# Optimization experiments

Measured on AMD Instinct MI355X. Metric: run time of the kernel, lower is better.

## Reference

```python
import jax, jax.numpy as jnp
import numpy as np

N = 50000      # nodes
E = 800000     # edges
IN = 32        # raw node feature dim
PE = 15        # laplacian PE dim (k)
HID = 128      # hidden
HEADS = 4
C = HID // HEADS
G = 64         # graphs in batch
L = 4          # num layers (shared weights!)


def setup_inputs() -> dict:
    key = jax.random.key(0)
    ks = jax.random.split(key, 24)
    s = 0.05
    p = lambda k, shape: jax.random.normal(k, shape, dtype=jnp.float32) * s
    inp = {
        "x": jax.random.normal(ks[0], (N, IN), dtype=jnp.float32),
        "edge_index": jax.random.randint(ks[1], (2, E), 0, N, dtype=jnp.int32),
        "batch": jnp.sort(jax.random.randint(ks[2], (N,), 0, G, dtype=jnp.int32)),
        "lap_pe": jax.random.normal(ks[3], (N, PE), dtype=jnp.float32),
        # node_in: Linear(IN+PE -> HID)
        "node_in_w": p(ks[4], (HID, IN + PE)), "node_in_b": p(ks[5], (HID,)),
        # shared TransformerConv params
        "Wq": p(ks[6], (HID, HID)), "bq": p(ks[7], (HID,)),
        "Wk": p(ks[8], (HID, HID)), "bk": p(ks[9], (HID,)),
        "Wv": p(ks[10], (HID, HID)), "bv": p(ks[11], (HID,)),
        "Wskip": p(ks[12], (HID, HID)), "bskip": p(ks[13], (HID,)),
        "Wbeta": p(ks[14], (1, 3 * HID)),  # bias=False in PyG
        # attentional aggregation gate: Linear(HID,HID)->ReLU->Linear(HID,1)
        "g1_w": p(ks[15], (HID, HID)), "g1_b": p(ks[16], (HID,)),
        "g2_w": p(ks[17], (1, HID)), "g2_b": p(ks[18], (1,)),
        # readout: Linear(HID,HID)->ReLU->Linear(HID,1)
        "r1_w": p(ks[19], (HID, HID)), "r1_b": p(ks[20], (HID,)),
        "r2_w": p(ks[21], (1, HID)), "r2_b": p(ks[22], (1,)),
    }
    return inp


def _transformer_conv(x, src, dst, Wq, bq, Wk, bk, Wv, bv, Wskip, bskip, Wbeta):
    # projections -> [N, HEADS, C]
    q = (x @ Wq.T + bq).reshape(N, HEADS, C)
    k = (x @ Wk.T + bk).reshape(N, HEADS, C)
    v = (x @ Wv.T + bv).reshape(N, HEADS, C)
    # edge attention logits: [E, HEADS]
    alpha = jnp.einsum('ehc,ehc->eh', q[dst], k[src]) / jnp.sqrt(jnp.float32(C))
    # segment softmax over destination node
    amax = jax.ops.segment_max(alpha, dst, num_segments=N)        # [N, HEADS]
    ex = jnp.exp(alpha - amax[dst])
    denom = jax.ops.segment_sum(ex, dst, num_segments=N)          # [N, HEADS]
    attn = ex / denom[dst]                                        # [E, HEADS]
    # weighted scatter-add of values
    msg = v[src] * attn[:, :, None]                               # [E, HEADS, C]
    out = jax.ops.segment_sum(msg, dst, num_segments=N).reshape(N, HID)
    # beta-gated skip connection (beta=True, root_weight=True)
    x_r = x @ Wskip.T + bskip
    beta = jax.nn.sigmoid(jnp.concatenate([out, x_r, out - x_r], axis=-1) @ Wbeta.T)
    return beta * x_r + (1.0 - beta) * out


def reference(x, edge_index, batch, lap_pe, node_in_w, node_in_b,
              Wq, bq, Wk, bk, Wv, bv, Wskip, bskip, Wbeta,
              g1_w, g1_b, g2_w, g2_b, r1_w, r1_b, r2_w, r2_b):
    src, dst = edge_index[0], edge_index[1]
    h = jnp.concatenate([x, lap_pe], axis=-1) @ node_in_w.T + node_in_b  # [N, HID]
    for _ in range(L):  # same conv instance reused -> shared weights
        h = jax.nn.relu(h + _transformer_conv(h, src, dst, Wq, bq, Wk, bk,
                                              Wv, bv, Wskip, bskip, Wbeta))
    # attentional aggregation over graphs
    gate = jax.nn.relu(h @ g1_w.T + g1_b) @ g2_w.T + g2_b                # [N, 1]
    gmax = jax.ops.segment_max(gate, batch, num_segments=G)
    gex = jnp.exp(gate - gmax[batch])
    gden = jax.ops.segment_sum(gex, batch, num_segments=G)
    w = gex / gden[batch]                                                # [N, 1]
    g = jax.ops.segment_sum(w * h, batch, num_segments=G)                # [G, HID]
    out = jax.nn.relu(g @ r1_w.T + r1_b) @ r2_w.T + r2_b                 # [G, 1]
    return out.squeeze(-1)
```

## Files before the change

kernel.cpp:

```cpp
#include <hip/hip_runtime.h>

#define NN 50000
#define EE 800000
#define INF 32
#define PEF 15
#define HID 128
#define GG 64
#define NLAYERS 4
#define NBLK 196

typedef __bf16 bf16;
typedef __attribute__((ext_vector_type(8))) bf16 bf16x8;
typedef __attribute__((ext_vector_type(4))) float f32x4;
typedef __attribute__((ext_vector_type(2))) float f32x2;

__device__ __forceinline__ float wave_allsum(float v) {
  #pragma unroll
  for (int off = 1; off < 64; off <<= 1) v += __shfl_xor(v, off);
  return v;
}

__device__ __forceinline__ float bflo(unsigned u) {
  return __builtin_bit_cast(float, u << 16);
}
__device__ __forceinline__ float bfhi(unsigned u) {
  return __builtin_bit_cast(float, u & 0xffff0000u);
}
__device__ __forceinline__ unsigned short f2bf(float v) {
  unsigned b = __builtin_bit_cast(unsigned, v);
  unsigned r = (b + 0x7fffu + ((b >> 16) & 1u)) >> 16;
  return (unsigned short)r;
}
__device__ __forceinline__ unsigned bfpack(float lo, float hi) {
  return (unsigned)f2bf(lo) | ((unsigned)f2bf(hi) << 16);
}
__device__ __forceinline__ unsigned fp8pack4(float a, float b, float c, float d) {
  unsigned lo = (unsigned)__builtin_amdgcn_cvt_pk_fp8_f32(a, b, 0, false) & 0xffffu;
  unsigned hi = (unsigned)__builtin_amdgcn_cvt_pk_fp8_f32(c, d, 0, false) & 0xffffu;
  return lo | (hi << 16);
}

__global__ void pack_weights_kernel(const float* __restrict__ Wq, const float* __restrict__ Wk,
                                    const float* __restrict__ Wv, const float* __restrict__ Ws,
                                    const float* __restrict__ bq, const float* __restrict__ bk,
                                    const float* __restrict__ bv, const float* __restrict__ bs,
                                    unsigned short* __restrict__ Wcatb, float* __restrict__ bcat) {
  int idx = blockIdx.x * blockDim.x + threadIdx.x;
  if (idx >= 512 * 128) return;
  int o = idx >> 7, j = idx & 127;
  int w = o >> 7, r = o & 127;
  const float* W = (w == 0) ? Wq : (w == 1) ? Wk : (w == 2) ? Wv : Ws;
  Wcatb[idx] = f2bf(W[r * 128 + j]);
  if (j == 0) {
    const float* b = (w == 0) ? bq : (w == 1) ? bk : (w == 2) ? bv : bs;
    bcat[o] = b[r];
  }
}

__global__ void pack_nwt_kernel(const float* __restrict__ niw, float* __restrict__ nwT) {
  int idx = blockIdx.x * blockDim.x + threadIdx.x;
  if (idx >= 47 * 128) return;
  int j = idx >> 7, o = idx & 127;
  nwT[j * 128 + o] = niw[o * 47 + j];
}

__global__ void pack_g1_kernel(const float* __restrict__ g1w, unsigned short* __restrict__ g1wb) {
  int idx = blockIdx.x * blockDim.x + threadIdx.x;
  if (idx >= 128 * 128) return;
  g1wb[idx] = f2bf(g1w[idx]);
}

__global__ __launch_bounds__(256) void nodein_kernel(const float* __restrict__ x,
    const float* __restrict__ pe, const float* __restrict__ nwT,
    const float* __restrict__ bias, float* __restrict__ h,
    unsigned short* __restrict__ hbf) {
  int wv = blockIdx.x * 4 + (threadIdx.x >> 6);
  if (wv >= NN) return;
  int lane = threadIdx.x & 63;
  float acc0 = bias[lane], acc1 = bias[64 + lane];
  const float* xr = x + (size_t)wv * INF;
  const float* pr = pe + (size_t)wv * PEF;
  #pragma unroll
  for (int j = 0; j < INF; j++) {
    float f = xr[j];
    acc0 += f * nwT[j * 128 + lane];
    acc1 += f * nwT[j * 128 + 64 + lane];
  }
  #pragma unroll
  for (int j = 0; j < PEF; j++) {
    float f = pr[j];
    acc0 += f * nwT[(INF + j) * 128 + lane];
    acc1 += f * nwT[(INF + j) * 128 + 64 + lane];
  }
  h[(size_t)wv * 128 + lane] = acc0;
  h[(size_t)wv * 128 + 64 + lane] = acc1;
  hbf[(size_t)wv * 128 + lane] = f2bf(acc0);
  hbf[(size_t)wv * 128 + 64 + lane] = f2bf(acc1);
}

__global__ void count_kernel(const int* __restrict__ dst, int* __restrict__ counts) {
  int e = blockIdx.x * blockDim.x + threadIdx.x;
  if (e >= EE) return;
  atomicAdd(&counts[dst[e]], 1);
}

__global__ __launch_bounds__(256) void bsum_kernel(const int* __restrict__ counts,
                                                   int* __restrict__ bsum) {
  int b = blockIdx.x, t = threadIdx.x;
  int i = b * 256 + t;
  int v = (i < NN) ? counts[i] : 0;
  #pragma unroll
  for (int off = 1; off < 64; off <<= 1) v += __shfl_xor(v, off);
  __shared__ int red[4];
  if ((t & 63) == 0) red[t >> 6] = v;
  __syncthreads();
  if (t == 0) bsum[b] = red[0] + red[1] + red[2] + red[3];
}

__global__ void bscan_kernel(const int* __restrict__ bsum, int* __restrict__ bbase) {
  int lane = threadIdx.x;
  int carry = 0;
  for (int c = 0; c < NBLK; c += 64) {
    int i = c + lane;
    int v = (i < NBLK) ? bsum[i] : 0;
    int x = v;
    #pragma unroll
    for (int off = 1; off < 64; off <<= 1) {
      int u = __shfl_up(x, off);
      if (lane >= off) x += u;
    }
    if (i < NBLK) bbase[i] = carry + x - v;
    carry += __shfl(x, 63);
  }
}

__global__ __launch_bounds__(256) void rowptr_kernel(const int* __restrict__ counts,
    const int* __restrict__ bbase, int* __restrict__ row_ptr, int* __restrict__ cursor) {
  int b = blockIdx.x, t = threadIdx.x;
  int lane = t & 63, wid = t >> 6;
  int i = b * 256 + t;
  int v = (i < NN) ? counts[i] : 0;
  int x = v;
  #pragma unroll
  for (int off = 1; off < 64; off <<= 1) {
    int u = __shfl_up(x, off);
    if (lane >= off) x += u;
  }
  __shared__ int wsum[4];
  if (lane == 63) wsum[wid] = x;
  __syncthreads();
  int offs = bbase[b];
  for (int k = 0; k < wid; k++) offs += wsum[k];
  int incl = offs + x;
  if (i < NN) { row_ptr[i + 1] = incl; cursor[i] = incl - v; }
  if (b == 0 && t == 0) row_ptr[0] = 0;
}

__global__ void scatter_kernel(const int* __restrict__ src, const int* __restrict__ dst,
                               int* __restrict__ cursor, int* __restrict__ srcs) {
  int e = blockIdx.x * blockDim.x + threadIdx.x;
  if (e >= EE) return;
  int d = dst[e];
  int p = atomicAdd(&cursor[d], 1);
  srcs[p] = src[e];
}

__global__ void gptr_kernel(const int* __restrict__ batch, int* __restrict__ gptr) {
  int g = threadIdx.x;
  if (g > GG) return;
  if (g == GG) { gptr[GG] = NN; return; }
  int lo = 0, hi = NN;
  while (lo < hi) {
    int mid = (lo + hi) >> 1;
    if (batch[mid] < g) lo = mid + 1; else hi = mid;
  }
  gptr[g] = lo;
}

__global__ __launch_bounds__(256) void gemm0_kernel(
    const bf16* __restrict__ A, const bf16* __restrict__ B,
    const float* __restrict__ bias, int M,
    unsigned short* __restrict__ qbb, unsigned char* __restrict__ kvb,
    unsigned short* __restrict__ xrbb) {
  __shared__ float lds[128 * 64];
  const int t = threadIdx.x;
  const int w = t >> 6, lane = t & 63;
  const int m0 = blockIdx.x * 128;
  const int by = blockIdx.y;
  const int n0 = by * 64;
  const int lrow = lane & 15, lk = (lane >> 4) * 8;
  int ra = m0 + w * 32 + lrow;      if (ra > M - 1) ra = M - 1;
  int rb = m0 + w * 32 + 16 + lrow; if (rb > M - 1) rb = M - 1;
  const bf16* a0p = A + (size_t)ra * 128 + lk;
  const bf16* a1p = A + (size_t)rb * 128 + lk;
  const bf16* bp  = B + (size_t)(n0 + lrow) * 128 + lk;
  f32x4 acc[2][4] = {};
  #pragma unroll
  for (int ks = 0; ks < 4; ks++) {
    bf16x8 a0 = *(const bf16x8*)(a0p + ks * 32);
    bf16x8 a1 = *(const bf16x8*)(a1p + ks * 32);
    #pragma unroll
    for (int nj = 0; nj < 4; nj++) {
      bf16x8 b = *(const bf16x8*)(bp + (size_t)nj * 2048 + ks * 32);
      acc[0][nj] = __builtin_amdgcn_mfma_f32_16x16x32_bf16(a0, b, acc[0][nj], 0, 0, 0);
      acc[1][nj] = __builtin_amdgcn_mfma_f32_16x16x32_bf16(a1, b, acc[1][nj], 0, 0, 0);
    }
  }
  const int rbase = (lane >> 4) * 4;
  #pragma unroll
  for (int mi = 0; mi < 2; mi++) {
    #pragma unroll
    for (int nj = 0; nj < 4; nj++) {
      #pragma unroll
      for (int r = 0; r < 4; r++) {
        int ml = w * 32 + mi * 16 + rbase + r;
        int col = nj * 16 + lrow;
        lds[ml * 64 + (col ^ ((ml & 7) << 2))] = acc[mi][nj][r] + bias[n0 + col];
      }
    }
  }
  __syncthreads();
  #pragma unroll
  for (int kk = 0; kk < 2; kk++) {
    int u = t + kk * 256;
    int r = u & 127, s = u >> 7;
    int m = m0 + r;
    float ff[16];
    #pragma unroll
    for (int j = 0; j < 4; j++) {
      int c = s * 16 + j * 4;
      *(float4*)(ff + j * 4) = *(const float4*)(lds + r * 64 + (c ^ ((r & 7) << 2)));
    }
    if (m < M) {
      int c0 = (by & 1) * 64 + s * 16;
      if (by < 2) {
        unsigned o[8];
        #pragma unroll
        for (int i = 0; i < 8; i++) o[i] = bfpack(ff[2 * i], ff[2 * i + 1]);
        uint4* dst = (uint4*)(qbb + (size_t)m * 128 + c0);
        dst[0] = *(uint4*)&o[0];
        dst[1] = *(uint4*)&o[4];
      } else if (by < 6) {
        unsigned o[4];
        #pragma unroll
        for (int i = 0; i < 4; i++)
          o[i] = fp8pack4(ff[4 * i], ff[4 * i + 1], ff[4 * i + 2], ff[4 * i + 3]);
        int cell = c0 >> 3;
        int voff = (by < 4) ? 0 : 8;
        unsigned char* bp8 = kvb + (size_t)m * 256;
        uint2 w0; w0.x = o[0]; w0.y = o[1];
        uint2 w1; w1.x = o[2]; w1.y = o[3];
        *(uint2*)(bp8 + cell * 16 + voff) = w0;
        *(uint2*)(bp8 + (cell + 1) * 16 + voff) = w1;
      } else {
        unsigned o[8];
        #pragma unroll
        for (int i = 0; i < 8; i++) o[i] = bfpack(ff[2 * i], ff[2 * i + 1]);
        uint4* dst = (uint4*)(xrbb + (size_t)m * 128 + c0);
        dst[0] = *(uint4*)&o[0];
        dst[1] = *(uint4*)&o[4];
      }
    }
  }
}

__global__ __launch_bounds__(512) void gemm1_gate_kernel(
    const bf16* __restrict__ A, const bf16* __restrict__ B,
    const float* __restrict__ b1, const float* __restrict__ g2w,
    const float* __restrict__ g2b, int M, float* __restrict__ gx) {
  const int w = threadIdx.x >> 6, lane = threadIdx.x & 63;
  const int m0 = blockIdx.x * 128 + w * 16;
  const int lrow = lane & 15, lk = (lane >> 4) * 8;
  int ra = m0 + lrow; if (ra > M - 1) ra = M - 1;
  const bf16* ap = A + (size_t)ra * 128 + lk;
  const bf16* bp = B + (size_t)lrow * 128 + lk;
  f32x4 acc[8] = {};
  #pragma unroll
  for (int ks = 0; ks < 4; ks++) {
    bf16x8 a = *(const bf16x8*)(ap + ks * 32);
    #pragma unroll
    for (int nj = 0; nj < 8; nj++) {
      bf16x8 b = *(const bf16x8*)(bp + (size_t)nj * 2048 + ks * 32);
      acc[nj] = __builtin_amdgcn_mfma_f32_16x16x32_bf16(a, b, acc[nj], 0, 0, 0);
    }
  }
  float g2v[8], b1v[8];
  #pragma unroll
  for (int nj = 0; nj < 8; nj++) {
    g2v[nj] = g2w[nj * 16 + lrow];
    b1v[nj] = b1[nj * 16 + lrow];
  }
  const float b2 = g2b[0];
  const int rbase = (lane >> 4) * 4;
  #pragma unroll
  for (int r = 0; r < 4; r++) {
    int m = m0 + rbase + r;
    float d = 0.f;
    #pragma unroll
    for (int nj = 0; nj < 8; nj++)
      d += fmaxf(acc[nj][r] + b1v[nj], 0.f) * g2v[nj];
    d += __shfl_xor(d, 1);
    d += __shfl_xor(d, 2);
    d += __shfl_xor(d, 4);
    d += __shfl_xor(d, 8);
    if (lrow == 0 && m < M) gx[m] = __expf(d + b2);
  }
}

__global__ __launch_bounds__(256) void attn_beta_kernel(
    const unsigned short* __restrict__ qbb,
    const unsigned char* __restrict__ kvb,
    const int* __restrict__ row_ptr, const int* __restrict__ srcs,
    const unsigned* __restrict__ xrb4,
    const float* __restrict__ Wbeta,
    float* __restrict__ h, unsigned* __restrict__ hbf4) {
  __shared__ float xlds[4][128];
  const int wid = threadIdx.x >> 6;
  const int wv = blockIdx.x * 4 + wid;
  const int lane = threadIdx.x & 63;
  const int sl = lane & 15;
  const int eg = lane >> 4;
  float qf[8];
  {
    bf16x8 qv = *(const bf16x8*)((const bf16*)qbb + (size_t)wv * 128 + sl * 8);
    #pragma unroll
    for (int j = 0; j < 8; j++) qf[j] = (float)qv[j];
  }
  const int e0 = row_ptr[wv], e1 = row_ptr[wv + 1];
  const float C = 0.25503486f;
  float dex = 0.f;
  float acc[8] = {0, 0, 0, 0, 0, 0, 0, 0};

#define PROC(cell, valid)                                                   \
  {                                                                         \
    f32x2 k0 = __builtin_amdgcn_cvt_pk_f32_fp8((cell).x, false);            \
    f32x2 k1 = __builtin_amdgcn_cvt_pk_f32_fp8((cell).x, true);             \
    f32x2 k2 = __builtin_amdgcn_cvt_pk_f32_fp8((cell).y, false);            \
    f32x2 k3 = __builtin_amdgcn_cvt_pk_f32_fp8((cell).y, true);             \
    float p = qf[0] * k0.x + qf[1] * k0.y + qf[2] * k1.x + qf[3] * k1.y     \
            + qf[4] * k2.x + qf[5] * k2.y + qf[6] * k3.x + qf[7] * k3.y;    \
    p += __shfl_xor(p, 1);                                                  \
    p += __shfl_xor(p, 2);                                                  \
    float ex = (valid) ? exp2f(p * C) : 0.f;                                \
    dex += ex;                                                              \
    f32x2 v0 = __builtin_amdgcn_cvt_pk_f32_fp8((cell).z, false);            \
    f32x2 v1 = __builtin_amdgcn_cvt_pk_f32_fp8((cell).z, true);             \
    f32x2 v2 = __builtin_amdgcn_cvt_pk_f32_fp8((cell).w, false);            \
    f32x2 v3 = __builtin_amdgcn_cvt_pk_f32_fp8((cell).w, true);             \
    acc[0] += ex * v0.x; acc[1] += ex * v0.y;                               \
    acc[2] += ex * v1.x; acc[3] += ex * v1.y;                               \
    acc[4] += ex * v2.x; acc[5] += ex * v2.y;                               \
    acc[6] += ex * v3.x; acc[7] += ex * v3.y;                               \
  }

  for (int base = e0; base < e1; base += 64) {
    int rem = e1 - base;
    int cnt = rem < 64 ? rem : 64;
    int mysrc = (lane < rem) ? srcs[base + lane] : 0;
    int i = 0;
    for (; i + 4 < cnt; i += 8) {
      int sea = __shfl(mysrc, i + eg);
      int seb = __shfl(mysrc, i + 4 + eg);
      uint4 ca = *(const uint4*)(kvb + (size_t)sea * 256 + sl * 16);
      uint4 cb = *(const uint4*)(kvb + (size_t)seb * 256 + sl * 16);
      PROC(ca, true);
      PROC(cb, (i + 4 + eg < cnt));
    }
    if (i < cnt) {
      int sea = __shfl(mysrc, i + eg);
      uint4 ca = *(const uint4*)(kvb + (size_t)sea * 256 + sl * 16);
      PROC(ca, (i + eg < cnt));
    }
  }
#undef PROC

  dex += __shfl_xor(dex, 16);
  dex += __shfl_xor(dex, 32);
  #pragma unroll
  for (int j = 0; j < 8; j++) {
    acc[j] += __shfl_xor(acc[j], 16);
    acc[j] += __shfl_xor(acc[j], 32);
  }
  float inv = (e1 > e0) ? 1.f / dex : 0.f;
  if (eg == 0) {
    #pragma unroll
    for (int j = 0; j < 8; j++) xlds[wid][sl * 8 + j] = acc[j] * inv;
  }
  __syncthreads();
  float ox = xlds[wid][2 * lane];
  float oy = xlds[wid][2 * lane + 1];
  unsigned xu = xrb4[(size_t)wv * 64 + lane];
  float xx = bflo(xu), xy = bfhi(xu);
  const float2* wb = (const float2*)Wbeta;
  float2 wo = wb[lane], wx = wb[64 + lane], wd = wb[128 + lane];
  float part = ox * wo.x + oy * wo.y + xx * wx.x + xy * wx.y
             + (ox - xx) * wd.x + (oy - xy) * wd.y;
  part = wave_allsum(part);
  float beta = 1.f / (1.f + __expf(-part));
  float2* hp = (float2*)(h + (size_t)wv * 128);
  float2 h2 = hp[lane];
  float r0 = fmaxf(h2.x + beta * xx + (1.f - beta) * ox, 0.f);
  float r1 = fmaxf(h2.y + beta * xy + (1.f - beta) * oy, 0.f);
  h2.x = r0; h2.y = r1;
  hp[lane] = h2;
  hbf4[(size_t)wv * 64 + lane] = bfpack(r0, r1);
}

__global__ __launch_bounds__(256) void gden_kernel(const float* __restrict__ gx,
    const int* __restrict__ gptr, float* __restrict__ gden) {
  int g = blockIdx.x, t = threadIdx.x;
  int n0 = gptr[g], n1 = gptr[g + 1];
  float s = 0.f;
  for (int n = n0 + t; n < n1; n += 256) s += gx[n];
  s = wave_allsum(s);
  __shared__ float red[4];
  if ((t & 63) == 0) red[t >> 6] = s;
  __syncthreads();
  if (t == 0) gden[g] = red[0] + red[1] + red[2] + red[3];
}

__global__ __launch_bounds__(128) void gagg_kernel(const float* __restrict__ gx,
    const float* __restrict__ h, const int* __restrict__ gptr,
    float* __restrict__ gfeat_raw) {
  int g = blockIdx.x;
  int c = blockIdx.y;
  int d = threadIdx.x;
  int n0 = gptr[g], n1 = gptr[g + 1];
  float acc = 0.f;
  for (int n = n0 + c; n < n1; n += 32) acc += gx[n] * h[(size_t)n * 128 + d];
  atomicAdd(&gfeat_raw[g * 128 + d], acc);
}

__global__ __launch_bounds__(128) void readout_kernel(const float* __restrict__ gfeat_raw,
    const float* __restrict__ gden,
    const float* __restrict__ r1w, const float* __restrict__ r1b,
    const float* __restrict__ r2w, const float* __restrict__ r2b,
    float* __restrict__ out) {
  int g = blockIdx.x;
  int u = threadIdx.x;
  __shared__ float sh[128];
  __shared__ float red[128];
  float dv = gden[g];
  float inv = (dv > 0.f) ? 1.f / dv : 0.f;
  sh[u] = gfeat_raw[g * 128 + u] * inv;
  __syncthreads();
  float tacc = r1b[u];
  for (int j = 0; j < 128; j++) tacc += sh[j] * r1w[u * 128 + j];
  tacc = fmaxf(tacc, 0.f);
  red[u] = tacc * r2w[u];
  __syncthreads();
  for (int off = 64; off > 0; off >>= 1) {
    if (u < off) red[u] += red[u + off];
    __syncthreads();
  }
  if (u == 0) out[g] = red[0] + r2b[0];
}

extern "C" void kernel_launch(void* const* d_in, const int* in_sizes, int n_in,
                              void* d_out, int out_size, void* d_ws, size_t ws_size,
                              hipStream_t stream) {
  (void)in_sizes; (void)n_in; (void)out_size; (void)ws_size;
  const float* x     = (const float*)d_in[0];
  const int*   ei    = (const int*)d_in[1];
  const int*   batch = (const int*)d_in[2];
  const float* pe    = (const float*)d_in[3];
  const float* niw   = (const float*)d_in[4];
  const float* nib   = (const float*)d_in[5];
  const float* Wq    = (const float*)d_in[6];
  const float* bq    = (const float*)d_in[7];
  const float* Wk    = (const float*)d_in[8];
  const float* bk    = (const float*)d_in[9];
  const float* Wv    = (const float*)d_in[10];
  const float* bv    = (const float*)d_in[11];
  const float* Wsk   = (const float*)d_in[12];
  const float* bsk   = (const float*)d_in[13];
  const float* Wbeta = (const float*)d_in[14];
  const float* g1w   = (const float*)d_in[15];
  const float* g1b   = (const float*)d_in[16];
  const float* g2w   = (const float*)d_in[17];
  const float* g2b   = (const float*)d_in[18];
  const float* r1w   = (const float*)d_in[19];
  const float* r1b   = (const float*)d_in[20];
  const float* r2w   = (const float*)d_in[21];
  const float* r2b   = (const float*)d_in[22];
  float* out = (float*)d_out;

  float* ws = (float*)d_ws;
  float* h     = ws; ws += (size_t)NN * 128;
  float* qbbf  = ws; ws += (size_t)NN * 64;
  float* kvbf  = ws; ws += (size_t)NN * 64;
  float* xrbf  = ws; ws += (size_t)NN * 64;
  float* hbff  = ws; ws += (size_t)NN * 64;
  float* Wcatf = ws; ws += 512 * 64;
  float* g1wbf = ws; ws += 128 * 64;
  float* bcat  = ws; ws += 512;
  float* nwT   = ws; ws += 47 * 128;
  float* gx    = ws; ws += NN;
  float* gfeat = ws; ws += GG * 128;
  float* gden  = ws; ws += GG;
  int* row_ptr = (int*)ws;
  int* counts  = row_ptr + (NN + 1);
  int* cursor  = counts + NN;
  int* srcs    = cursor + NN;
  int* gptr    = srcs + EE;
  int* bsum    = gptr + (GG + 1);
  int* bbase   = bsum + 256;

  unsigned short* qbb   = (unsigned short*)qbbf;
  unsigned char*  kvb   = (unsigned char*)kvbf;
  unsigned short* xrbb  = (unsigned short*)xrbf;
  unsigned short* hbf   = (unsigned short*)hbff;
  unsigned short* Wcatb = (unsigned short*)Wcatf;
  unsigned short* g1wb  = (unsigned short*)g1wbf;
  const int* src = ei;
  const int* dst = ei + EE;

  hipMemsetAsync(counts, 0, NN * sizeof(int), stream);
  hipMemsetAsync(gfeat, 0, GG * 128 * sizeof(float), stream);
  pack_weights_kernel<<<(512 * 128 + 255) / 256, 256, 0, stream>>>(
      Wq, Wk, Wv, Wsk, bq, bk, bv, bsk, Wcatb, bcat);
  pack_nwt_kernel<<<(47 * 128 + 255) / 256, 256, 0, stream>>>(niw, nwT);
  pack_g1_kernel<<<(128 * 128 + 255) / 256, 256, 0, stream>>>(g1w, g1wb);
  nodein_kernel<<<12500, 256, 0, stream>>>(x, pe, nwT, nib, h, hbf);
  count_kernel<<<(EE + 255) / 256, 256, 0, stream>>>(dst, counts);
  bsum_kernel<<<NBLK, 256, 0, stream>>>(counts, bsum);
  bscan_kernel<<<1, 64, 0, stream>>>(bsum, bbase);
  rowptr_kernel<<<NBLK, 256, 0, stream>>>(counts, bbase, row_ptr, cursor);
  scatter_kernel<<<(EE + 255) / 256, 256, 0, stream>>>(src, dst, cursor, srcs);
  gptr_kernel<<<1, 128, 0, stream>>>(batch, gptr);

  const int MB0 = (NN + 127) / 128;
  for (int l = 0; l < NLAYERS; l++) {
    gemm0_kernel<<<dim3(MB0, 8), 256, 0, stream>>>(
        (const bf16*)hbf, (const bf16*)Wcatb, bcat, NN, qbb, kvb, xrbb);
    attn_beta_kernel<<<12500, 256, 0, stream>>>(
        qbb, kvb, row_ptr, srcs, (const unsigned*)xrbb, Wbeta, h, (unsigned*)hbf);
  }

  gemm1_gate_kernel<<<MB0, 512, 0, stream>>>(
      (const bf16*)hbf, (const bf16*)g1wb, g1b, g2w, g2b, NN, gx);
  gden_kernel<<<GG, 256, 0, stream>>>(gx, gptr, gden);
  gagg_kernel<<<dim3(GG, 32), 128, 0, stream>>>(gx, h, gptr, gfeat);
  readout_kernel<<<GG, 128, 0, stream>>>(gfeat, gden, r1w, r1b, r2w, r2b, out);
}
```

Before: 581.5 us.

## Replace scalar node-input projection with packed bf16 MFMA GEMM

The per-node scalar FMA projection of concatenated raw features and positional encodings is replaced by two kernels. One packs x and lap_pe into a zero-padded 64-wide bf16 row per node, and one runs an MFMA 16x16x32 GEMM against a padded bf16 weight matrix. The GEMM stages results through swizzled LDS so it can write coalesced fp32 h and bf16 hbf. This removes per-lane redundant weight loads and scalar FMAs. In exchange it adds an extra kernel and an intermediate buffer, and it drops the projection inputs from fp32 to bf16 precision.

```diff
diff --git a/kernel.cpp b/kernel.cpp
--- a/kernel.cpp
+++ b/kernel.cpp
@@ -57,11 +57,11 @@
   }
 }
 
-__global__ void pack_nwt_kernel(const float* __restrict__ niw, float* __restrict__ nwT) {
+__global__ void pack_nwtb_kernel(const float* __restrict__ niw, unsigned short* __restrict__ nwtb) {
   int idx = blockIdx.x * blockDim.x + threadIdx.x;
-  if (idx >= 47 * 128) return;
-  int j = idx >> 7, o = idx & 127;
-  nwT[j * 128 + o] = niw[o * 47 + j];
+  if (idx >= 128 * 64) return;
+  int n = idx >> 6, j = idx & 63;
+  nwtb[idx] = (j < INF + PEF) ? f2bf(niw[n * (INF + PEF) + j]) : (unsigned short)0;
 }
 
 __global__ void pack_g1_kernel(const float* __restrict__ g1w, unsigned short* __restrict__ g1wb) {
@@ -70,32 +70,96 @@
   g1wb[idx] = f2bf(g1w[idx]);
 }
 
-__global__ __launch_bounds__(256) void nodein_kernel(const float* __restrict__ x,
-    const float* __restrict__ pe, const float* __restrict__ nwT,
-    const float* __restrict__ bias, float* __restrict__ h,
-    unsigned short* __restrict__ hbf) {
-  int wv = blockIdx.x * 4 + (threadIdx.x >> 6);
-  if (wv >= NN) return;
-  int lane = threadIdx.x & 63;
-  float acc0 = bias[lane], acc1 = bias[64 + lane];
-  const float* xr = x + (size_t)wv * INF;
-  const float* pr = pe + (size_t)wv * PEF;
-  #pragma unroll
-  for (int j = 0; j < INF; j++) {
-    float f = xr[j];
-    acc0 += f * nwT[j * 128 + lane];
-    acc1 += f * nwT[j * 128 + 64 + lane];
-  }
-  #pragma unroll
-  for (int j = 0; j < PEF; j++) {
-    float f = pr[j];
-    acc0 += f * nwT[(INF + j) * 128 + lane];
-    acc1 += f * nwT[(INF + j) * 128 + 64 + lane];
-  }
-  h[(size_t)wv * 128 + lane] = acc0;
-  h[(size_t)wv * 128 + 64 + lane] = acc1;
-  hbf[(size_t)wv * 128 + lane] = f2bf(acc0);
-  hbf[(size_t)wv * 128 + 64 + lane] = f2bf(acc1);
+__global__ __launch_bounds__(256) void xpe_pack_kernel(const float* __restrict__ x,
+    const float* __restrict__ pe, unsigned* __restrict__ xpeb4) {
+  int n = blockIdx.x * 256 + threadIdx.x;
+  if (n >= NN) return;
+  unsigned ou[32];
+  const float4* xr = (const float4*)(x + (size_t)n * INF);
+  #pragma unroll
+  for (int i = 0; i < 8; i++) {
+    float4 v = xr[i];
+    ou[2 * i] = bfpack(v.x, v.y);
+    ou[2 * i + 1] = bfpack(v.z, v.w);
+  }
+  const float* pr = pe + (size_t)n * PEF;
+  float p[16];
+  #pragma unroll
+  for (int i = 0; i < PEF; i++) p[i] = pr[i];
+  p[15] = 0.f;
+  #pragma unroll
+  for (int i = 0; i < 8; i++) ou[16 + i] = bfpack(p[2 * i], p[2 * i + 1]);
+  #pragma unroll
+  for (int i = 24; i < 32; i++) ou[i] = 0u;
+  unsigned* dst = xpeb4 + (size_t)n * 32;
+  #pragma unroll
+  for (int i = 0; i < 8; i++) ((uint4*)dst)[i] = *(uint4*)&ou[4 * i];
+}
+
+__global__ __launch_bounds__(256) void nodein_gemm_kernel(
+    const bf16* __restrict__ A, const bf16* __restrict__ B,
+    const float* __restrict__ bias, int M,
+    float* __restrict__ h, unsigned* __restrict__ hbf4) {
+  __shared__ float lds[128 * 64];
+  const int t = threadIdx.x;
+  const int w = t >> 6, lane = t & 63;
+  const int m0 = blockIdx.x * 128;
+  const int n0 = blockIdx.y * 64;
+  const int lrow = lane & 15, lk = (lane >> 4) * 8;
+  int ra = m0 + w * 32 + lrow;      if (ra > M - 1) ra = M - 1;
+  int rb = m0 + w * 32 + 16 + lrow; if (rb > M - 1) rb = M - 1;
+  const bf16* a0p = A + (size_t)ra * 64 + lk;
+  const bf16* a1p = A + (size_t)rb * 64 + lk;
+  const bf16* bp  = B + (size_t)(n0 + lrow) * 64 + lk;
+  f32x4 acc[2][4] = {};
+  #pragma unroll
+  for (int ks = 0; ks < 2; ks++) {
+    bf16x8 a0 = *(const bf16x8*)(a0p + ks * 32);
+    bf16x8 a1 = *(const bf16x8*)(a1p + ks * 32);
+    #pragma unroll
+    for (int nj = 0; nj < 4; nj++) {
+      bf16x8 b = *(const bf16x8*)(bp + (size_t)nj * 1024 + ks * 32);
+      acc[0][nj] = __builtin_amdgcn_mfma_f32_16x16x32_bf16(a0, b, acc[0][nj], 0, 0, 0);
+      acc[1][nj] = __builtin_amdgcn_mfma_f32_16x16x32_bf16(a1, b, acc[1][nj], 0, 0, 0);
+    }
+  }
+  const int rbase = (lane >> 4) * 4;
+  #pragma unroll
+  for (int mi = 0; mi < 2; mi++) {
+    #pragma unroll
+    for (int nj = 0; nj < 4; nj++) {
+      #pragma unroll
+      for (int r = 0; r < 4; r++) {
+        int ml = w * 32 + mi * 16 + rbase + r;
+        int col = nj * 16 + lrow;
+        lds[ml * 64 + (col ^ ((ml & 7) << 2))] = acc[mi][nj][r] + bias[n0 + col];
+      }
+    }
+  }
+  __syncthreads();
+  #pragma unroll
+  for (int kk = 0; kk < 2; kk++) {
+    int u = t + kk * 256;
+    int r = u & 127, s = u >> 7;
+    int m = m0 + r;
+    if (m >= M) continue;
+    float ff[16];
+    #pragma unroll
+    for (int j = 0; j < 4; j++) {
+      int c = s * 16 + j * 4;
+      *(float4*)(ff + j * 4) = *(const float4*)(lds + r * 64 + (c ^ ((r & 7) << 2)));
+    }
+    int c0 = n0 + s * 16;
+    float4* hp = (float4*)(h + (size_t)m * 128 + c0);
+    #pragma unroll
+    for (int j = 0; j < 4; j++) hp[j] = *(float4*)(ff + j * 4);
+    unsigned o[8];
+    #pragma unroll
+    for (int i = 0; i < 8; i++) o[i] = bfpack(ff[2 * i], ff[2 * i + 1]);
+    uint4* hb = (uint4*)(hbf4 + (size_t)m * 64 + (c0 >> 1));
+    hb[0] = *(uint4*)&o[0];
+    hb[1] = *(uint4*)&o[4];
+  }
 }
 
 __global__ void count_kernel(const int* __restrict__ dst, int* __restrict__ counts) {
@@ -491,10 +555,11 @@
   float* kvbf  = ws; ws += (size_t)NN * 64;
   float* xrbf  = ws; ws += (size_t)NN * 64;
   float* hbff  = ws; ws += (size_t)NN * 64;
+  float* xpebf = ws; ws += (size_t)NN * 32;
   float* Wcatf = ws; ws += 512 * 64;
   float* g1wbf = ws; ws += 128 * 64;
+  float* nwtbf = ws; ws += 128 * 32;
   float* bcat  = ws; ws += 512;
-  float* nwT   = ws; ws += 47 * 128;
   float* gx    = ws; ws += NN;
   float* gfeat = ws; ws += GG * 128;
   float* gden  = ws; ws += GG;
@@ -512,6 +577,7 @@
   unsigned short* hbf   = (unsigned short*)hbff;
   unsigned short* Wcatb = (unsigned short*)Wcatf;
   unsigned short* g1wb  = (unsigned short*)g1wbf;
+  unsigned short* nwtb  = (unsigned short*)nwtbf;
   const int* src = ei;
   const int* dst = ei + EE;
 
@@ -519,9 +585,9 @@
   hipMemsetAsync(gfeat, 0, GG * 128 * sizeof(float), stream);
   pack_weights_kernel<<<(512 * 128 + 255) / 256, 256, 0, stream>>>(
       Wq, Wk, Wv, Wsk, bq, bk, bv, bsk, Wcatb, bcat);
-  pack_nwt_kernel<<<(47 * 128 + 255) / 256, 256, 0, stream>>>(niw, nwT);
+  pack_nwtb_kernel<<<(128 * 64 + 255) / 256, 256, 0, stream>>>(niw, nwtb);
   pack_g1_kernel<<<(128 * 128 + 255) / 256, 256, 0, stream>>>(g1w, g1wb);
-  nodein_kernel<<<12500, 256, 0, stream>>>(x, pe, nwT, nib, h, hbf);
+  xpe_pack_kernel<<<NBLK, 256, 0, stream>>>(x, pe, (unsigned*)xpebf);
   count_kernel<<<(EE + 255) / 256, 256, 0, stream>>>(dst, counts);
   bsum_kernel<<<NBLK, 256, 0, stream>>>(counts, bsum);
   bscan_kernel<<<1, 64, 0, stream>>>(bsum, bbase);
@@ -530,6 +596,9 @@
   gptr_kernel<<<1, 128, 0, stream>>>(batch, gptr);
 
   const int MB0 = (NN + 127) / 128;
+  nodein_gemm_kernel<<<dim3(MB0, 2), 256, 0, stream>>>(
+      (const bf16*)xpebf, (const bf16*)nwtb, nib, NN, h, (unsigned*)hbf);
+
   for (int l = 0; l < NLAYERS; l++) {
     gemm0_kernel<<<dim3(MB0, 8), 256, 0, stream>>>(
         (const bf16*)hbf, (const bf16*)Wcatb, bcat, NN, qbb, kvb, xrbb);
```

Result: faster. 552.7 us (-5.0%).
